# Kernel tuning notes

Measured on AMD Instinct MI355X. Metric: run time of the kernel, lower is better.

The kernel has to match this reference:

```python
import jax, jax.numpy as jnp
import numpy as np

HIGH_T = 0.75
LOW_T = 0.25
EPS = 1e-6


def quantize_four_val(w):
    # {-1, -0.5, 0, 0.5, 1} banding per thresholds (0 band for |w| <= LOW_T)
    return jnp.where(w > HIGH_T, 1.0,
           jnp.where(w > LOW_T, 0.5,
           jnp.where(w < -HIGH_T, -1.0,
           jnp.where(w < -LOW_T, -0.5, 0.0))))


def setup_inputs() -> dict:
    key = jax.random.key(0)
    k1, k2, k3, k4 = jax.random.split(key, 4)
    B, S, D_IN, D_OUT = 4, 2048, 2048, 2048
    x_real = jax.random.normal(k1, (B, S, D_IN), dtype=jnp.float32)
    x_imag = jax.random.normal(k2, (B, S, D_IN), dtype=jnp.float32)
    # unit-normal weights so all four quantization levels are exercised
    weight_re = jax.random.normal(k3, (D_OUT, D_IN), dtype=jnp.float32)
    weight_im = jax.random.normal(k4, (D_OUT, D_IN), dtype=jnp.float32)
    gamma = jnp.ones((2 * D_IN,), dtype=jnp.float32)
    beta = jnp.zeros((2 * D_IN,), dtype=jnp.float32)
    return {"x_real": x_real, "x_imag": x_imag, "weight_re": weight_re,
            "weight_im": weight_im, "gamma": gamma, "beta": beta}


def reference(x_real, x_imag, weight_re, weight_im, gamma, beta):
    d = x_real.shape[-1]
    # LayerNorm over concatenated [real, imag] last dim (2*d)
    x_cat = jnp.concatenate([x_real, x_imag], axis=-1)
    mu = jnp.mean(x_cat, axis=-1, keepdims=True)
    var = jnp.var(x_cat, axis=-1, keepdims=True)
    norm = (x_cat - mu) * jax.lax.rsqrt(var + EPS) * gamma + beta
    nr, ni = norm[..., :d], norm[..., d:]
    # STE: forward uses quantized weights
    qw_re = quantize_four_val(weight_re)
    qw_im = quantize_four_val(weight_im)
    s_re = jnp.mean(jnp.abs(weight_re))
    s_im = jnp.mean(jnp.abs(weight_im))
    y_real = nr @ qw_re.T - ni @ qw_im.T
    y_imag = nr @ qw_im.T + ni @ qw_re.T
    return (y_real * s_re, y_imag * s_im)
```

## Files before the change

kernel.cpp:

```cpp
#include <hip/hip_runtime.h>
#include <hip/hip_bf16.h>

constexpr int D_IN  = 2048;
constexpr int D_OUT = 2048;
constexpr int GM = 4 * 2048;
constexpr int GK = 2 * D_IN;
constexpr int GN = 2 * D_OUT;

typedef __attribute__((ext_vector_type(8))) short bf16x8;
typedef __attribute__((ext_vector_type(4))) float f32x4;

constexpr int QB = 1024;

__device__ inline unsigned short q4bits(float w) {
    if (w >  0.75f) return 0x3F80;
    if (w >  0.25f) return 0x3F00;
    if (w < -0.75f) return 0xBF80;
    if (w < -0.25f) return 0xBF00;
    return 0;
}

__device__ inline unsigned short bf16b(float x) {
    __hip_bfloat16 h = __float2bfloat16(x);
    unsigned short u;
    __builtin_memcpy(&u, &h, 2);
    return u;
}

__global__ __launch_bounds__(256) void prep_kernel(
        const float* __restrict__ xr, const float* __restrict__ xi,
        const float* __restrict__ gamma, const float* __restrict__ beta,
        unsigned short* __restrict__ A,
        const float* __restrict__ wre, const float* __restrict__ wim,
        unsigned short* __restrict__ wq, float* __restrict__ partial) {
    __shared__ float red[8];
    __shared__ float smu, srs;

    if (blockIdx.x >= GM) {
        int qb = blockIdx.x - GM;
        float a = 0.f, b = 0.f;
        int tid = qb * 256 + threadIdx.x;
        const float4* wre4 = (const float4*)wre;
        const float4* wim4 = (const float4*)wim;
        for (int c = 0; c < 4; c++) {
            int f4i = tid + c * (QB * 256);
            int idx = f4i * 4;
            int o = idx >> 11;
            int k = idx & (D_IN - 1);
            float4 r = wre4[f4i];
            float4 im = wim4[f4i];
            a += fabsf(r.x) + fabsf(r.y) + fabsf(r.z) + fabsf(r.w);
            b += fabsf(im.x) + fabsf(im.y) + fabsf(im.z) + fabsf(im.w);
            ushort4 qre, qim, nim;
            qre.x = q4bits(r.x);  qre.y = q4bits(r.y);  qre.z = q4bits(r.z);  qre.w = q4bits(r.w);
            qim.x = q4bits(im.x); qim.y = q4bits(im.y); qim.z = q4bits(im.z); qim.w = q4bits(im.w);
            nim.x = qim.x ^ 0x8000; nim.y = qim.y ^ 0x8000;
            nim.z = qim.z ^ 0x8000; nim.w = qim.w ^ 0x8000;
            *(ushort4*)(wq + (size_t)o * GK + k)                  = qre;
            *(ushort4*)(wq + (size_t)o * GK + D_IN + k)           = nim;
            *(ushort4*)(wq + (size_t)(D_OUT + o) * GK + k)        = qim;
            *(ushort4*)(wq + (size_t)(D_OUT + o) * GK + D_IN + k) = qre;
        }
        for (int off = 32; off; off >>= 1) {
            a += __shfl_down(a, off, 64);
            b += __shfl_down(b, off, 64);
        }
        int lane = threadIdx.x & 63, wv = threadIdx.x >> 6;
        if (lane == 0) { red[wv] = a; red[4 + wv] = b; }
        __syncthreads();
        if (threadIdx.x == 0) {
            partial[qb]      = red[0] + red[1] + red[2] + red[3];
            partial[QB + qb] = red[4] + red[5] + red[6] + red[7];
        }
        return;
    }

    int m = blockIdx.x;
    int t = threadIdx.x;
    const float4* r4 = (const float4*)(xr + (size_t)m * D_IN);
    const float4* i4 = (const float4*)(xi + (size_t)m * D_IN);
    float4 vr[2], vi[2];
    float s = 0.f, ss = 0.f;
    for (int c = 0; c < 2; c++) {
        float4 v = r4[t + c * 256];
        vr[c] = v;
        s  += v.x + v.y + v.z + v.w;
        ss += v.x * v.x + v.y * v.y + v.z * v.z + v.w * v.w;
        v = i4[t + c * 256];
        vi[c] = v;
        s  += v.x + v.y + v.z + v.w;
        ss += v.x * v.x + v.y * v.y + v.z * v.z + v.w * v.w;
    }
    for (int off = 32; off; off >>= 1) {
        s  += __shfl_down(s, off, 64);
        ss += __shfl_down(ss, off, 64);
    }
    int lane = t & 63, wv = t >> 6;
    if (lane == 0) { red[wv] = s; red[4 + wv] = ss; }
    __syncthreads();
    if (t == 0) {
        float S  = red[0] + red[1] + red[2] + red[3];
        float SS = red[4] + red[5] + red[6] + red[7];
        float mu  = S * (1.0f / 4096.0f);
        float var = SS * (1.0f / 4096.0f) - mu * mu;
        smu = mu;
        srs = rsqrtf(var + 1e-6f);
    }
    __syncthreads();
    float mu = smu, rs = srs;
    const float4* g4 = (const float4*)gamma;
    const float4* b4 = (const float4*)beta;
    ushort4* Arow = (ushort4*)(A + (size_t)m * GK);
    for (int c = 0; c < 2; c++) {
        int k4 = t + c * 256;
        float4 g = g4[k4], b = b4[k4];
        float4 v = vr[c];
        ushort4 o;
        o.x = bf16b((v.x - mu) * rs * g.x + b.x);
        o.y = bf16b((v.y - mu) * rs * g.y + b.y);
        o.z = bf16b((v.z - mu) * rs * g.z + b.z);
        o.w = bf16b((v.w - mu) * rs * g.w + b.w);
        Arow[k4] = o;
        g = g4[512 + k4]; b = b4[512 + k4];
        v = vi[c];
        o.x = bf16b((v.x - mu) * rs * g.x + b.x);
        o.y = bf16b((v.y - mu) * rs * g.y + b.y);
        o.z = bf16b((v.z - mu) * rs * g.z + b.z);
        o.w = bf16b((v.w - mu) * rs * g.w + b.w);
        Arow[512 + k4] = o;
    }
}

__global__ __launch_bounds__(256, 2) void gemm_kernel(
        const unsigned short* __restrict__ A,
        const unsigned short* __restrict__ Wq,
        const float* __restrict__ partial,
        float* __restrict__ out) {
    constexpr int BM = 128, BN = 128, BK = 64;
    __shared__ unsigned short lsA[BM * BK];
    __shared__ unsigned short lsB[BN * BK];
    __shared__ float sred[8];
    __shared__ float s_scale[2];
    int n0 = blockIdx.x * BN;
    int m0 = blockIdx.y * BM;
    int t = threadIdx.x, lane = t & 63, wave = t >> 6;
    int wm = (wave >> 1) * 64;
    int wn = (wave & 1) * 64;
    int quad = lane >> 4, r = lane & 15;
    int srow = lane >> 3;
    int scol = ((lane & 7) ^ srow) * 8;
    int csw0 = ((quad ^ (r & 7)) * 8);

    {
        float a = 0.f, b = 0.f;
        for (int i = t; i < QB; i += 256) { a += partial[i]; b += partial[QB + i]; }
        for (int off = 32; off; off >>= 1) {
            a += __shfl_down(a, off, 64);
            b += __shfl_down(b, off, 64);
        }
        if (lane == 0) { sred[wave] = a; sred[4 + wave] = b; }
        __syncthreads();
        if (t == 0) {
            s_scale[0] = (sred[0] + sred[1] + sred[2] + sred[3]) * (1.0f / (2048.0f * 2048.0f));
            s_scale[1] = (sred[4] + sred[5] + sred[6] + sred[7]) * (1.0f / (2048.0f * 2048.0f));
        }
    }

    f32x4 acc[4][4] = {};

    for (int k0 = 0; k0 < GK; k0 += BK) {
        for (int i = 0; i < 4; i++) {
            int row = i * 32 + wave * 8;
            const unsigned short* gp = A + (size_t)(m0 + row + srow) * GK + k0 + scol;
            unsigned short* lp = lsA + row * BK;
            __builtin_amdgcn_global_load_lds(
                (const __attribute__((address_space(1))) void*)(const void*)gp,
                (__attribute__((address_space(3))) void*)(void*)lp, 16, 0, 0);
        }
        for (int i = 0; i < 4; i++) {
            int row = i * 32 + wave * 8;
            const unsigned short* gp = Wq + (size_t)(n0 + row + srow) * GK + k0 + scol;
            unsigned short* lp = lsB + row * BK;
            __builtin_amdgcn_global_load_lds(
                (const __attribute__((address_space(1))) void*)(const void*)gp,
                (__attribute__((address_space(3))) void*)(void*)lp, 16, 0, 0);
        }
        __syncthreads();
        for (int ks = 0; ks < 2; ks++) {
            bf16x8 af[4], bfr[4];
            const short* pa = (const short*)lsA;
            const short* pb = (const short*)lsB;
            int coff = csw0 ^ (ks * 32);
            for (int i = 0; i < 4; i++)
                af[i] = *(const bf16x8*)(pa + (wm + i * 16 + r) * BK + coff);
            for (int j = 0; j < 4; j++)
                bfr[j] = *(const bf16x8*)(pb + (wn + j * 16 + r) * BK + coff);
            for (int i = 0; i < 4; i++)
                for (int j = 0; j < 4; j++)
                    acc[i][j] = __builtin_amdgcn_mfma_f32_16x16x32_bf16(
                        af[i], bfr[j], acc[i][j], 0, 0, 0);
        }
        __syncthreads();
    }

    float scale;
    float* obase;
    int ncol0;
    if (n0 < D_OUT) { scale = s_scale[0]; obase = out;                      ncol0 = n0; }
    else            { scale = s_scale[1]; obase = out + (size_t)GM * D_OUT; ncol0 = n0 - D_OUT; }

    for (int i = 0; i < 4; i++)
        for (int j = 0; j < 4; j++) {
            int mrow = m0 + wm + i * 16 + quad * 4;
            int ncol = ncol0 + wn + j * 16 + r;
            for (int reg = 0; reg < 4; reg++)
                obase[(size_t)(mrow + reg) * D_OUT + ncol] = acc[i][j][reg] * scale;
        }
}

extern "C" void kernel_launch(void* const* d_in, const int* in_sizes, int n_in,
                              void* d_out, int out_size, void* d_ws, size_t ws_size,
                              hipStream_t stream) {
    const float* xr    = (const float*)d_in[0];
    const float* xi    = (const float*)d_in[1];
    const float* wre   = (const float*)d_in[2];
    const float* wim   = (const float*)d_in[3];
    const float* gamma = (const float*)d_in[4];
    const float* beta  = (const float*)d_in[5];
    float* out = (float*)d_out;

    unsigned short* A  = (unsigned short*)d_ws;
    unsigned short* Wq = (unsigned short*)((char*)d_ws + (size_t)GM * GK * 2);
    float* partial = (float*)((char*)d_ws + (size_t)GM * GK * 2 + (size_t)GN * GK * 2);

    prep_kernel<<<GM + QB, 256, 0, stream>>>(xr, xi, gamma, beta, A,
                                             wre, wim, Wq, partial);
    gemm_kernel<<<dim3(GN / 128, GM / 128), 256, 0, stream>>>(A, Wq, partial, out);
}
```

Baseline: 478.7 us.

## Enlarge GEMM block tile to 256x128 with 8x4 MFMA fragments per wave

Doubles the M dimension of each GEMM workgroup tile so each wave computes a 128x64 output slice with 32 accumulators. This raises operand reuse from LDS and halves global B-tile reloads per output. It costs many more accumulator registers and more LDS per block, which risks spills or lower occupancy. The prep kernel is refactored into helper functions with a shared scratch array.

```diff
diff --git a/kernel.cpp b/kernel.cpp
--- a/kernel.cpp
+++ b/kernel.cpp
@@ -27,56 +27,10 @@
     return u;
 }
 
-__global__ __launch_bounds__(256) void prep_kernel(
+__device__ __forceinline__ void ln_unit(int m, int t,
         const float* __restrict__ xr, const float* __restrict__ xi,
         const float* __restrict__ gamma, const float* __restrict__ beta,
-        unsigned short* __restrict__ A,
-        const float* __restrict__ wre, const float* __restrict__ wim,
-        unsigned short* __restrict__ wq, float* __restrict__ partial) {
-    __shared__ float red[8];
-    __shared__ float smu, srs;
-
-    if (blockIdx.x >= GM) {
-        int qb = blockIdx.x - GM;
-        float a = 0.f, b = 0.f;
-        int tid = qb * 256 + threadIdx.x;
-        const float4* wre4 = (const float4*)wre;
-        const float4* wim4 = (const float4*)wim;
-        for (int c = 0; c < 4; c++) {
-            int f4i = tid + c * (QB * 256);
-            int idx = f4i * 4;
-            int o = idx >> 11;
-            int k = idx & (D_IN - 1);
-            float4 r = wre4[f4i];
-            float4 im = wim4[f4i];
-            a += fabsf(r.x) + fabsf(r.y) + fabsf(r.z) + fabsf(r.w);
-            b += fabsf(im.x) + fabsf(im.y) + fabsf(im.z) + fabsf(im.w);
-            ushort4 qre, qim, nim;
-            qre.x = q4bits(r.x);  qre.y = q4bits(r.y);  qre.z = q4bits(r.z);  qre.w = q4bits(r.w);
-            qim.x = q4bits(im.x); qim.y = q4bits(im.y); qim.z = q4bits(im.z); qim.w = q4bits(im.w);
-            nim.x = qim.x ^ 0x8000; nim.y = qim.y ^ 0x8000;
-            nim.z = qim.z ^ 0x8000; nim.w = qim.w ^ 0x8000;
-            *(ushort4*)(wq + (size_t)o * GK + k)                  = qre;
-            *(ushort4*)(wq + (size_t)o * GK + D_IN + k)           = nim;
-            *(ushort4*)(wq + (size_t)(D_OUT + o) * GK + k)        = qim;
-            *(ushort4*)(wq + (size_t)(D_OUT + o) * GK + D_IN + k) = qre;
-        }
-        for (int off = 32; off; off >>= 1) {
-            a += __shfl_down(a, off, 64);
-            b += __shfl_down(b, off, 64);
-        }
-        int lane = threadIdx.x & 63, wv = threadIdx.x >> 6;
-        if (lane == 0) { red[wv] = a; red[4 + wv] = b; }
-        __syncthreads();
-        if (threadIdx.x == 0) {
-            partial[qb]      = red[0] + red[1] + red[2] + red[3];
-            partial[QB + qb] = red[4] + red[5] + red[6] + red[7];
-        }
-        return;
-    }
-
-    int m = blockIdx.x;
-    int t = threadIdx.x;
+        unsigned short* __restrict__ A, float* shf) {
     const float4* r4 = (const float4*)(xr + (size_t)m * D_IN);
     const float4* i4 = (const float4*)(xi + (size_t)m * D_IN);
     float4 vr[2], vi[2];
@@ -96,18 +50,18 @@
         ss += __shfl_down(ss, off, 64);
     }
     int lane = t & 63, wv = t >> 6;
-    if (lane == 0) { red[wv] = s; red[4 + wv] = ss; }
+    if (lane == 0) { shf[wv] = s; shf[4 + wv] = ss; }
     __syncthreads();
     if (t == 0) {
-        float S  = red[0] + red[1] + red[2] + red[3];
-        float SS = red[4] + red[5] + red[6] + red[7];
+        float S  = shf[0] + shf[1] + shf[2] + shf[3];
+        float SS = shf[4] + shf[5] + shf[6] + shf[7];
         float mu  = S * (1.0f / 4096.0f);
         float var = SS * (1.0f / 4096.0f) - mu * mu;
-        smu = mu;
-        srs = rsqrtf(var + 1e-6f);
+        shf[8] = mu;
+        shf[9] = rsqrtf(var + 1e-6f);
     }
     __syncthreads();
-    float mu = smu, rs = srs;
+    float mu = shf[8], rs = shf[9];
     const float4* g4 = (const float4*)gamma;
     const float4* b4 = (const float4*)beta;
     ushort4* Arow = (ushort4*)(A + (size_t)m * GK);
@@ -131,21 +85,73 @@
     }
 }
 
+__device__ __forceinline__ void quant_unit(int qb, int t,
+        const float* __restrict__ wre, const float* __restrict__ wim,
+        unsigned short* __restrict__ wq, float* __restrict__ partial,
+        float* shf) {
+    float a = 0.f, b = 0.f;
+    int tid = qb * 256 + t;
+    const float4* wre4 = (const float4*)wre;
+    const float4* wim4 = (const float4*)wim;
+    for (int c = 0; c < 4; c++) {
+        int f4i = tid + c * (QB * 256);
+        int idx = f4i * 4;
+        int o = idx >> 11;
+        int k = idx & (D_IN - 1);
+        float4 r = wre4[f4i];
+        float4 im = wim4[f4i];
+        a += fabsf(r.x) + fabsf(r.y) + fabsf(r.z) + fabsf(r.w);
+        b += fabsf(im.x) + fabsf(im.y) + fabsf(im.z) + fabsf(im.w);
+        ushort4 qre, qim, nim;
+        qre.x = q4bits(r.x);  qre.y = q4bits(r.y);  qre.z = q4bits(r.z);  qre.w = q4bits(r.w);
+        qim.x = q4bits(im.x); qim.y = q4bits(im.y); qim.z = q4bits(im.z); qim.w = q4bits(im.w);
+        nim.x = qim.x ^ 0x8000; nim.y = qim.y ^ 0x8000;
+        nim.z = qim.z ^ 0x8000; nim.w = qim.w ^ 0x8000;
+        *(ushort4*)(wq + (size_t)o * GK + k)                  = qre;
+        *(ushort4*)(wq + (size_t)o * GK + D_IN + k)           = nim;
+        *(ushort4*)(wq + (size_t)(D_OUT + o) * GK + k)        = qim;
+        *(ushort4*)(wq + (size_t)(D_OUT + o) * GK + D_IN + k) = qre;
+    }
+    for (int off = 32; off; off >>= 1) {
+        a += __shfl_down(a, off, 64);
+        b += __shfl_down(b, off, 64);
+    }
+    int lane = t & 63, wv = t >> 6;
+    if (lane == 0) { shf[wv] = a; shf[4 + wv] = b; }
+    __syncthreads();
+    if (t == 0) {
+        partial[qb]      = shf[0] + shf[1] + shf[2] + shf[3];
+        partial[QB + qb] = shf[4] + shf[5] + shf[6] + shf[7];
+    }
+}
+
+__global__ __launch_bounds__(256) void prep_kernel(
+        const float* __restrict__ xr, const float* __restrict__ xi,
+        const float* __restrict__ gamma, const float* __restrict__ beta,
+        unsigned short* __restrict__ A,
+        const float* __restrict__ wre, const float* __restrict__ wim,
+        unsigned short* __restrict__ wq, float* __restrict__ partial) {
+    __shared__ float shf[10];
+    if (blockIdx.x >= GM) {
+        quant_unit(blockIdx.x - GM, threadIdx.x, wre, wim, wq, partial, shf);
+        return;
+    }
+    ln_unit(blockIdx.x, threadIdx.x, xr, xi, gamma, beta, A, shf);
+}
+
 __global__ __launch_bounds__(256, 2) void gemm_kernel(
         const unsigned short* __restrict__ A,
         const unsigned short* __restrict__ Wq,
         const float* __restrict__ partial,
         float* __restrict__ out) {
-    constexpr int BM = 128, BN = 128, BK = 64;
+    constexpr int BM = 256, BN = 128, BK = 64;
     __shared__ unsigned short lsA[BM * BK];
     __shared__ unsigned short lsB[BN * BK];
-    __shared__ float sred[8];
-    __shared__ float s_scale[2];
+    __shared__ float shf[10];
     int n0 = blockIdx.x * BN;
     int m0 = blockIdx.y * BM;
     int t = threadIdx.x, lane = t & 63, wave = t >> 6;
-    int wm = (wave >> 1) * 64;
-    int wn = (wave & 1) * 64;
+    int wr = wave >> 1, wc = wave & 1;
     int quad = lane >> 4, r = lane & 15;
     int srow = lane >> 3;
     int scol = ((lane & 7) ^ srow) * 8;
@@ -158,18 +164,18 @@
             a += __shfl_down(a, off, 64);
             b += __shfl_down(b, off, 64);
         }
-        if (lane == 0) { sred[wave] = a; sred[4 + wave] = b; }
+        if (lane == 0) { shf[wave] = a; shf[4 + wave] = b; }
         __syncthreads();
         if (t == 0) {
-            s_scale[0] = (sred[0] + sred[1] + sred[2] + sred[3]) * (1.0f / (2048.0f * 2048.0f));
-            s_scale[1] = (sred[4] + sred[5] + sred[6] + sred[7]) * (1.0f / (2048.0f * 2048.0f));
-        }
-    }
-
-    f32x4 acc[4][4] = {};
+            shf[8] = (shf[0] + shf[1] + shf[2] + shf[3]) * (1.0f / (2048.0f * 2048.0f));
+            shf[9] = (shf[4] + shf[5] + shf[6] + shf[7]) * (1.0f / (2048.0f * 2048.0f));
+        }
+    }
+
+    f32x4 acc[8][4] = {};
 
     for (int k0 = 0; k0 < GK; k0 += BK) {
-        for (int i = 0; i < 4; i++) {
+        for (int i = 0; i < 8; i++) {
             int row = i * 32 + wave * 8;
             const unsigned short* gp = A + (size_t)(m0 + row + srow) * GK + k0 + scol;
             unsigned short* lp = lsA + row * BK;
@@ -187,18 +193,22 @@
         }
         __syncthreads();
         for (int ks = 0; ks < 2; ks++) {
-            bf16x8 af[4], bfr[4];
+            bf16x8 af[8], bfr[4];
             const short* pa = (const short*)lsA;
             const short* pb = (const short*)lsB;
             int coff = csw0 ^ (ks * 32);
-            for (int i = 0; i < 4; i++)
-                af[i] = *(const bf16x8*)(pa + (wm + i * 16 + r) * BK + coff);
-            for (int j = 0; j < 4; j++)
-                bfr[j] = *(const bf16x8*)(pb + (wn + j * 16 + r) * BK + coff);
-            for (int i = 0; i < 4; i++)
-                for (int j = 0; j < 4; j++)
-                    acc[i][j] = __builtin_amdgcn_mfma_f32_16x16x32_bf16(
-                        af[i], bfr[j], acc[i][j], 0, 0, 0);
+            #pragma unroll
+            for (int f = 0; f < 8; f++)
+                af[f] = *(const bf16x8*)(pa + (wr * 128 + f * 16 + r) * BK + coff);
+            #pragma unroll
+            for (int g = 0; g < 4; g++)
+                bfr[g] = *(const bf16x8*)(pb + (wc * 64 + g * 16 + r) * BK + coff);
+            #pragma unroll
+            for (int f = 0; f < 8; f++)
+                #pragma unroll
+                for (int g = 0; g < 4; g++)
+                    acc[f][g] = __builtin_amdgcn_mfma_f32_16x16x32_bf16(
+                        af[f], bfr[g], acc[f][g], 0, 0, 0);
         }
         __syncthreads();
     }
@@ -206,15 +216,18 @@
     float scale;
     float* obase;
     int ncol0;
-    if (n0 < D_OUT) { scale = s_scale[0]; obase = out;                      ncol0 = n0; }
-    else            { scale = s_scale[1]; obase = out + (size_t)GM * D_OUT; ncol0 = n0 - D_OUT; }
-
-    for (int i = 0; i < 4; i++)
-        for (int j = 0; j < 4; j++) {
-            int mrow = m0 + wm + i * 16 + quad * 4;
-            int ncol = ncol0 + wn + j * 16 + r;
+    if (n0 < D_OUT) { scale = shf[8]; obase = out;                      ncol0 = n0; }
+    else            { scale = shf[9]; obase = out + (size_t)GM * D_OUT; ncol0 = n0 - D_OUT; }
+
+    #pragma unroll
+    for (int f = 0; f < 8; f++)
+        #pragma unroll
+        for (int g = 0; g < 4; g++) {
+            int mrow = m0 + wr * 128 + f * 16 + quad * 4;
+            int ncol = ncol0 + wc * 64 + g * 16 + r;
+            #pragma unroll
             for (int reg = 0; reg < 4; reg++)
-                obase[(size_t)(mrow + reg) * D_OUT + ncol] = acc[i][j][reg] * scale;
+                obase[(size_t)(mrow + reg) * D_OUT + ncol] = acc[f][g][reg] * scale;
         }
 }
 
@@ -235,5 +248,5 @@
 
     prep_kernel<<<GM + QB, 256, 0, stream>>>(xr, xi, gamma, beta, A,
                                              wre, wim, Wq, partial);
-    gemm_kernel<<<dim3(GN / 128, GM / 128), 256, 0, stream>>>(A, Wq, partial, out);
-}
+    gemm_kernel<<<dim3(GN / 128, GM / 256), 256, 0, stream>>>(A, Wq, partial, out);
+}
```

New measurement: 472.5 us. About the same (-1.3%).
